# Performance work log

Measured on AMD Instinct MI355X. Metric: run time of the kernel, lower is better.

The kernel has to match this reference:

```python
import jax, jax.numpy as jnp
import numpy as np

N, E, D, R = 50000, 625000, 128, 200
BN_EPS = 1e-5


def setup_inputs() -> dict:
    key = jax.random.key(0)
    ks = jax.random.split(key, 16)
    x = jax.random.normal(ks[0], (N, D), dtype=jnp.float32)
    r_feats = jax.random.normal(ks[1], (R, D), dtype=jnp.float32)
    src = jax.random.randint(ks[2], (E,), 0, N, dtype=jnp.int32)
    dst = jax.random.randint(ks[3], (E,), 0, N, dtype=jnp.int32)
    etype = jax.random.randint(ks[4], (E,), 0, R, dtype=jnp.int32)
    norm = jax.random.uniform(ks[5], (E, 1), dtype=jnp.float32)
    out_edges_mask = jax.random.randint(ks[6], (E,), 0, 2) == 1
    in_edges_mask = jnp.logical_not(out_edges_mask)  # masks partition edges
    s = 1.0 / np.sqrt(D)
    def lin(k):
        kw, kb = jax.random.split(k)
        return (jax.random.uniform(kw, (D, D), jnp.float32, -s, s),
                jax.random.uniform(kb, (D,), jnp.float32, -s, s))
    W_O_w, W_O_b = lin(ks[7])
    W_I_w, W_I_b = lin(ks[8])
    W_S_w, W_S_b = lin(ks[9])
    W_R_w, W_R_b = lin(ks[10])
    loop_rel = jax.random.normal(ks[11], (1, D), dtype=jnp.float32) * s  # xavier-ish
    bn_gamma = jnp.ones((D,), jnp.float32)
    bn_beta = jnp.zeros((D,), jnp.float32)
    return {"x": x, "r_feats": r_feats, "src": src, "dst": dst, "etype": etype,
            "norm": norm, "in_edges_mask": in_edges_mask, "out_edges_mask": out_edges_mask,
            "W_O_w": W_O_w, "W_O_b": W_O_b, "W_I_w": W_I_w, "W_I_b": W_I_b,
            "W_S_w": W_S_w, "W_S_b": W_S_b, "W_R_w": W_R_w, "W_R_b": W_R_b,
            "loop_rel": loop_rel, "bn_gamma": bn_gamma, "bn_beta": bn_beta}


def reference(x, r_feats, src, dst, etype, norm, in_edges_mask, out_edges_mask,
              W_O_w, W_O_b, W_I_w, W_I_b, W_S_w, W_S_b, W_R_w, W_R_b,
              loop_rel, bn_gamma, bn_beta):
    # r_feats with self-loop relation appended: [R+1, D]
    r_ext = jnp.concatenate([r_feats, loop_rel], axis=0)
    # per-edge relation feature scaled by norm: [E, D]
    e_h = r_ext[etype] * norm
    # compose (sub): u_sub_e -> src feature minus edge feature
    comp_h = x[src] - e_h
    # per-direction linear projections, selected by the edge partition masks
    h_O = comp_h @ W_O_w.T + W_O_b
    h_I = comp_h @ W_I_w.T + W_I_b
    new_comp_h = jnp.where(out_edges_mask[:, None], h_O, h_I)
    # scatter-sum messages to destination nodes: [N, D]
    agg = jax.ops.segment_sum(new_comp_h, dst, num_segments=x.shape[0])
    # self-loop branch (sub with loop relation)
    comp_h_s = x - r_ext[-1]
    n_out = (comp_h_s @ W_S_w.T + W_S_b + agg) * (1.0 / 3.0)  # dropout in eval mode
    # BatchNorm1d (training-mode batch stats, biased variance)
    mean = jnp.mean(n_out, axis=0)
    var = jnp.mean((n_out - mean) ** 2, axis=0)
    n_out = (n_out - mean) * jax.lax.rsqrt(var + BN_EPS) * bn_gamma + bn_beta
    n_out = jnp.tanh(n_out)
    r_out = r_ext @ W_R_w.T + W_R_b
    return n_out, r_out[:-1]
```

## Files before the change

kernel.cpp:

```cpp
#include <hip/hip_runtime.h>
#include <cstddef>

#define N_NODES 50000
#define N_EDGES 625000
#define DIM     128
#define R_REL   200
#define BN_EPS  1e-5f
#define SLOTS   64
#define ND4     ((N_NODES * DIM) / 4)
#define R4      ((R_REL * DIM) / 4)

#define NB_FILL  2442
#define NB_CONV  3200
#define PREP_BASE (NB_FILL + NB_CONV)
#define NB_PREP  128
#define ROUT_BASE (PREP_BASE + NB_PREP)
#define NB_ROUT  100
#define NB_TOTAL (ROUT_BASE + NB_ROUT)

typedef __bf16 bf16x8 __attribute__((ext_vector_type(8)));
typedef float  f32x4  __attribute__((ext_vector_type(4)));

__device__ __forceinline__ float bfu2f(unsigned int hi16) {
    return __uint_as_float(hi16);
}
__device__ __forceinline__ unsigned int f2bfr(float f) {
    unsigned int u = __float_as_uint(f);
    return (u + 0x7fffu + ((u >> 16) & 1u)) >> 16;
}

__global__ __launch_bounds__(256) void init0_kernel(
    int* __restrict__ cnt,
    const unsigned char* __restrict__ in_m, const unsigned char* __restrict__ out_m,
    int* __restrict__ flag) {
    int gid = blockIdx.x * 256 + threadIdx.x;
    if (gid < N_NODES) cnt[gid] = 0;
    if (blockIdx.x == 0) {
        int ok = (((int)in_m[threadIdx.x] + (int)out_m[threadIdx.x]) == 1) ? 1 : 0;
        __shared__ int sred[4];
        unsigned long long b = __ballot(ok);
        if ((threadIdx.x & 63) == 0) sred[threadIdx.x >> 6] = (b == ~0ULL) ? 1 : 0;
        __syncthreads();
        if (threadIdx.x == 0) *flag = sred[0] & sred[1] & sred[2] & sred[3];
    }
}

__global__ __launch_bounds__(256) void fused_front_kernel(
    const int* __restrict__ dst, const int* __restrict__ src,
    const int* __restrict__ et, const float* __restrict__ norm,
    const void* __restrict__ omask, const int* __restrict__ flag,
    int* __restrict__ cnt, uint2* __restrict__ erec,
    const float* __restrict__ x, ushort* __restrict__ xb,
    const float* __restrict__ rf, ushort* __restrict__ rb,
    const float* __restrict__ WO, const float* __restrict__ WI,
    const float* __restrict__ WS, const float* __restrict__ loop,
    const float* __restrict__ bS, const float* __restrict__ bO,
    const float* __restrict__ bI, ushort* __restrict__ Wb,
    float* __restrict__ bias0, float* __restrict__ bO3, float* __restrict__ bI3,
    float* __restrict__ colsum, float* __restrict__ colsq,
    const float* __restrict__ WR, const float* __restrict__ bR,
    float* __restrict__ rout) {
    __shared__ float smem[256];
    int b = blockIdx.x, t = threadIdx.x;

    if (b < NB_FILL) {
        int e = b * 256 + t;
        if (e >= N_EDGES) return;
        int fl = *flag;
        bool m = fl ? (((const unsigned char*)omask)[e] != 0)
                    : (((const int*)omask)[e] != 0);
        int d = dst[e];
        int k = atomicAdd(&cnt[d], 1);
        if (k < SLOTS) {
            unsigned w0 = (unsigned)src[e] | ((unsigned)et[e] << 16) | (m ? 0x80000000u : 0u);
            erec[(size_t)d * SLOTS + k] = make_uint2(w0, (unsigned)__float_as_int(norm[e]));
        }
    } else if (b < PREP_BASE) {
        int cgid = (b - NB_FILL) * 256 + t;
        for (int i = cgid; i < ND4; i += NB_CONV * 256) {
            float4 v = ((const float4*)x)[i];
            ushort4 o;
            o.x = (ushort)f2bfr(v.x); o.y = (ushort)f2bfr(v.y);
            o.z = (ushort)f2bfr(v.z); o.w = (ushort)f2bfr(v.w);
            ((ushort4*)xb)[i] = o;
        }
        if (cgid < R4) {
            float4 v = ((const float4*)rf)[cgid];
            ushort4 o;
            o.x = (ushort)f2bfr(v.x); o.y = (ushort)f2bfr(v.y);
            o.z = (ushort)f2bfr(v.z); o.w = (ushort)f2bfr(v.w);
            ((ushort4*)rb)[cgid] = o;
        }
    } else if (b < ROUT_BASE) {
        int f = b - PREP_BASE;
        const float third = 1.0f / 3.0f;
        for (int k = t; k < 384; k += 256) {
            float w;
            if (k < 128)      w = WS[f * DIM + k];
            else if (k < 256) w = WO[f * DIM + (k - 128)];
            else              w = WI[f * DIM + (k - 256)];
            Wb[f * 384 + k] = (ushort)f2bfr(w * third);
        }
        if (t < 128) smem[t] = loop[t] * WS[f * DIM + t];
        __syncthreads();
        for (int off = 64; off; off >>= 1) {
            if (t < off) smem[t] += smem[t + off];
            __syncthreads();
        }
        if (t == 0) bias0[f] = (bS[f] - smem[0]) * third;
        if (t == 1) bO3[f] = bO[f] * third;
        if (t == 2) bI3[f] = bI[f] * third;
        if (f == 0 && t >= 128) { colsum[t - 128] = 0.f; colsq[t - 128] = 0.f; }
    } else {
        float* row2 = smem;
        int rloc = t >> 7, f = t & 127;
        int r = (b - ROUT_BASE) * 2 + rloc;
        row2[rloc * 128 + f] = rf[r * DIM + f];
        __syncthreads();
        float acc = bR[f];
        for (int k = 0; k < DIM; ++k) acc += row2[rloc * 128 + k] * WR[f * DIM + k];
        rout[r * DIM + f] = acc;
    }
}

#define AGG_CALC(EX, EY, XW, RW)                                   \
    {                                                              \
        float nm = __uint_as_float(EY);                            \
        float fm = (float)((EX) >> 31);                            \
        float x0 = bfu2f((XW) << 16), x1 = bfu2f((XW) & 0xffff0000u); \
        float r0 = bfu2f((RW) << 16), r1 = bfu2f((RW) & 0xffff0000u); \
        float v0 = __builtin_fmaf(-nm, r0, x0);                    \
        float v1 = __builtin_fmaf(-nm, r1, x1);                    \
        aT0 += v0; aT1 += v1;                                      \
        aO0 = __builtin_fmaf(fm, v0, aO0);                         \
        aO1 = __builtin_fmaf(fm, v1, aO1);                         \
        cOf += fm;                                                 \
    }

__global__ __launch_bounds__(256, 8) void aggregate_kernel(
    const unsigned int* __restrict__ xb,
    const unsigned int* __restrict__ rb,
    const uint2* __restrict__ erec,
    const int* __restrict__ cnt,
    unsigned int* __restrict__ S_Ob, unsigned int* __restrict__ S_Ib,
    float* __restrict__ cntO, float* __restrict__ cntI) {
    int wv = threadIdx.x >> 6;
    unsigned lane = threadIdx.x & 63;
    int n = blockIdx.x * 4 + wv;
    if (n >= N_NODES) return;
    int deg = cnt[n];
    deg = deg < SLOTS ? deg : SLOTS;
    int beg = n * SLOTS, end = beg + deg;

    float aT0 = 0.f, aT1 = 0.f, aO0 = 0.f, aO1 = 0.f, cOf = 0.f;

    int j = beg;
    for (; j + 7 < end; j += 8) {
        uint4 q01 = *(const uint4*)(erec + j);
        uint4 q23 = *(const uint4*)(erec + j + 2);
        uint4 q45 = *(const uint4*)(erec + j + 4);
        uint4 q67 = *(const uint4*)(erec + j + 6);
        unsigned xw0 = xb[((q01.x & 0xffffu) << 6) + lane];
        unsigned rw0 = rb[(((q01.x >> 16) & 0x7fffu) << 6) + lane];
        unsigned xw1 = xb[((q01.z & 0xffffu) << 6) + lane];
        unsigned rw1 = rb[(((q01.z >> 16) & 0x7fffu) << 6) + lane];
        unsigned xw2 = xb[((q23.x & 0xffffu) << 6) + lane];
        unsigned rw2 = rb[(((q23.x >> 16) & 0x7fffu) << 6) + lane];
        unsigned xw3 = xb[((q23.z & 0xffffu) << 6) + lane];
        unsigned rw3 = rb[(((q23.z >> 16) & 0x7fffu) << 6) + lane];
        unsigned xw4 = xb[((q45.x & 0xffffu) << 6) + lane];
        unsigned rw4 = rb[(((q45.x >> 16) & 0x7fffu) << 6) + lane];
        unsigned xw5 = xb[((q45.z & 0xffffu) << 6) + lane];
        unsigned rw5 = rb[(((q45.z >> 16) & 0x7fffu) << 6) + lane];
        unsigned xw6 = xb[((q67.x & 0xffffu) << 6) + lane];
        unsigned rw6 = rb[(((q67.x >> 16) & 0x7fffu) << 6) + lane];
        unsigned xw7 = xb[((q67.z & 0xffffu) << 6) + lane];
        unsigned rw7 = rb[(((q67.z >> 16) & 0x7fffu) << 6) + lane];
        AGG_CALC(q01.x, q01.y, xw0, rw0)
        AGG_CALC(q01.z, q01.w, xw1, rw1)
        AGG_CALC(q23.x, q23.y, xw2, rw2)
        AGG_CALC(q23.z, q23.w, xw3, rw3)
        AGG_CALC(q45.x, q45.y, xw4, rw4)
        AGG_CALC(q45.z, q45.w, xw5, rw5)
        AGG_CALC(q67.x, q67.y, xw6, rw6)
        AGG_CALC(q67.z, q67.w, xw7, rw7)
    }
    if (j + 3 < end) {
        uint4 q01 = *(const uint4*)(erec + j);
        uint4 q23 = *(const uint4*)(erec + j + 2);
        unsigned xw0 = xb[((q01.x & 0xffffu) << 6) + lane];
        unsigned rw0 = rb[(((q01.x >> 16) & 0x7fffu) << 6) + lane];
        unsigned xw1 = xb[((q01.z & 0xffffu) << 6) + lane];
        unsigned rw1 = rb[(((q01.z >> 16) & 0x7fffu) << 6) + lane];
        unsigned xw2 = xb[((q23.x & 0xffffu) << 6) + lane];
        unsigned rw2 = rb[(((q23.x >> 16) & 0x7fffu) << 6) + lane];
        unsigned xw3 = xb[((q23.z & 0xffffu) << 6) + lane];
        unsigned rw3 = rb[(((q23.z >> 16) & 0x7fffu) << 6) + lane];
        AGG_CALC(q01.x, q01.y, xw0, rw0)
        AGG_CALC(q01.z, q01.w, xw1, rw1)
        AGG_CALC(q23.x, q23.y, xw2, rw2)
        AGG_CALC(q23.z, q23.w, xw3, rw3)
        j += 4;
    }
    if (j + 1 < end) {
        uint4 q01 = *(const uint4*)(erec + j);
        unsigned xw0 = xb[((q01.x & 0xffffu) << 6) + lane];
        unsigned rw0 = rb[(((q01.x >> 16) & 0x7fffu) << 6) + lane];
        unsigned xw1 = xb[((q01.z & 0xffffu) << 6) + lane];
        unsigned rw1 = rb[(((q01.z >> 16) & 0x7fffu) << 6) + lane];
        AGG_CALC(q01.x, q01.y, xw0, rw0)
        AGG_CALC(q01.z, q01.w, xw1, rw1)
        j += 2;
    }
    if (j < end) {
        uint2 e0 = erec[j];
        unsigned xw0 = xb[((e0.x & 0xffffu) << 6) + lane];
        unsigned rw0 = rb[(((e0.x >> 16) & 0x7fffu) << 6) + lane];
        AGG_CALC(e0.x, e0.y, xw0, rw0)
    }

    float aI0 = aT0 - aO0, aI1 = aT1 - aO1;
    S_Ob[((unsigned)n << 6) + lane] = f2bfr(aO0) | (f2bfr(aO1) << 16);
    S_Ib[((unsigned)n << 6) + lane] = f2bfr(aI0) | (f2bfr(aI1) << 16);
    if (lane == 0) { cntO[n] = cOf; cntI[n] = (float)deg - cOf; }
}

__global__ __launch_bounds__(256, 4) void gemm_kernel(
    const ushort* __restrict__ xb, const ushort* __restrict__ S_Ob,
    const ushort* __restrict__ S_Ib, const ushort* __restrict__ Wb,
    const float* __restrict__ bias0, const float* __restrict__ bO3,
    const float* __restrict__ bI3, const float* __restrict__ cntO,
    const float* __restrict__ cntI, float* __restrict__ y,
    float* __restrict__ colsum, float* __restrict__ colsq) {
    __shared__ ushort Bs[128][136];
    __shared__ float redS[4][128];
    __shared__ float redQ[4][128];

    int tid = threadIdx.x;
    int wv = tid >> 6, lane = tid & 63;
    int cl = lane & 15, kg = lane >> 4;
    int wrow0 = blockIdx.x * 64 + wv * 16;

    f32x4 acc[8];
#pragma unroll
    for (int cf = 0; cf < 8; ++cf) acc[cf] = (f32x4){0.f, 0.f, 0.f, 0.f};

    int rowA = wrow0 + cl;
    int rowc = rowA < N_NODES ? rowA : N_NODES - 1;
    const ushort* Abase[3] = {xb, S_Ob, S_Ib};

    for (int kq = 0; kq < 3; ++kq) {
        __syncthreads();
#pragma unroll
        for (int j = 0; j < 8; ++j) {
            int i = tid + j * 256;
            int col = i >> 4, k8 = (i & 15) << 3;
            uint4 w = *(const uint4*)(Wb + (size_t)col * 384 + kq * 128 + k8);
            *(uint4*)&Bs[col][k8] = w;
        }
        const ushort* Ap0 = Abase[kq] + (size_t)rowc * 128 + kg * 8;
        uint4 a4[4];
#pragma unroll
        for (int ks = 0; ks < 4; ++ks) a4[ks] = *(const uint4*)(Ap0 + ks * 32);
        __syncthreads();
#pragma unroll
        for (int ks = 0; ks < 4; ++ks) {
            bf16x8 af = __builtin_bit_cast(bf16x8, a4[ks]);
#pragma unroll
            for (int cf = 0; cf < 8; ++cf) {
                bf16x8 bv = __builtin_bit_cast(bf16x8,
                    *(const uint4*)&Bs[cf * 16 + cl][ks * 32 + kg * 8]);
                acc[cf] = __builtin_amdgcn_mfma_f32_16x16x32_bf16(af, bv, acc[cf], 0, 0, 0);
            }
        }
    }

    float b0a[8], boa[8], bia[8];
#pragma unroll
    for (int cf = 0; cf < 8; ++cf) {
        int col = cf * 16 + cl;
        b0a[cf] = bias0[col]; boa[cf] = bO3[col]; bia[cf] = bI3[col];
    }
    float cOv[4], cIv[4]; int rows[4]; bool rv[4];
#pragma unroll
    for (int r = 0; r < 4; ++r) {
        int row = wrow0 + kg * 4 + r;
        rows[r] = row; rv[r] = row < N_NODES;
        cOv[r] = rv[r] ? cntO[row] : 0.f;
        cIv[r] = rv[r] ? cntI[row] : 0.f;
    }
    float ps[8], pq[8];
#pragma unroll
    for (int cf = 0; cf < 8; ++cf) {
        float s = 0.f, q = 0.f;
        int col = cf * 16 + cl;
#pragma unroll
        for (int r = 0; r < 4; ++r) {
            if (rv[r]) {
                float v = acc[cf][r] + b0a[cf] + cOv[r] * boa[cf] + cIv[r] * bia[cf];
                y[(size_t)rows[r] * DIM + col] = v;
                s += v; q += v * v;
            }
        }
        s += __shfl_xor(s, 16);
        s += __shfl_xor(s, 32);
        q += __shfl_xor(q, 16);
        q += __shfl_xor(q, 32);
        ps[cf] = s; pq[cf] = q;
    }
    if (kg == 0) {
#pragma unroll
        for (int cf = 0; cf < 8; ++cf) {
            redS[wv][cf * 16 + cl] = ps[cf];
            redQ[wv][cf * 16 + cl] = pq[cf];
        }
    }
    __syncthreads();
    if (tid < 128) {
        float s = redS[0][tid] + redS[1][tid] + redS[2][tid] + redS[3][tid];
        float q = redQ[0][tid] + redQ[1][tid] + redQ[2][tid] + redQ[3][tid];
        atomicAdd(colsum + tid, s);
        atomicAdd(colsq + tid, q);
    }
}

__global__ __launch_bounds__(256) void bn_apply_kernel(
    float* __restrict__ y, const float* __restrict__ colsum, const float* __restrict__ colsq,
    const float* __restrict__ gamma, const float* __restrict__ beta) {
    __shared__ __align__(16) float sc[DIM];
    __shared__ __align__(16) float sh[DIM];
    int tid = threadIdx.x;
    if (tid < DIM) {
        float mean = colsum[tid] * (1.0f / N_NODES);
        float var  = colsq[tid] * (1.0f / N_NODES) - mean * mean;
        float s = rsqrtf(var + BN_EPS) * gamma[tid];
        sc[tid] = s;
        sh[tid] = beta[tid] - mean * s;
    }
    __syncthreads();
    const int total4 = N_NODES * 32;
    for (int i = blockIdx.x * 256 + tid; i < total4; i += gridDim.x * 256) {
        float4 s4 = ((const float4*)sc)[i & 31];
        float4 h4 = ((const float4*)sh)[i & 31];
        float4 v = ((float4*)y)[i];
        v.x = tanhf(v.x * s4.x + h4.x);
        v.y = tanhf(v.y * s4.y + h4.y);
        v.z = tanhf(v.z * s4.z + h4.z);
        v.w = tanhf(v.w * s4.w + h4.w);
        ((float4*)y)[i] = v;
    }
}

extern "C" void kernel_launch(void* const* d_in, const int* in_sizes, int n_in,
                              void* d_out, int out_size, void* d_ws, size_t ws_size,
                              hipStream_t stream) {
    const float* x        = (const float*)d_in[0];
    const float* r_feats  = (const float*)d_in[1];
    const int*   src      = (const int*)d_in[2];
    const int*   dst      = (const int*)d_in[3];
    const int*   etype    = (const int*)d_in[4];
    const float* norm     = (const float*)d_in[5];
    const void*  in_mask  = d_in[6];
    const void*  out_mask = d_in[7];
    const float* W_O_w    = (const float*)d_in[8];
    const float* W_O_b    = (const float*)d_in[9];
    const float* W_I_w    = (const float*)d_in[10];
    const float* W_I_b    = (const float*)d_in[11];
    const float* W_S_w    = (const float*)d_in[12];
    const float* W_S_b    = (const float*)d_in[13];
    const float* W_R_w    = (const float*)d_in[14];
    const float* W_R_b    = (const float*)d_in[15];
    const float* loop_rel = (const float*)d_in[16];
    const float* bn_gamma = (const float*)d_in[17];
    const float* bn_beta  = (const float*)d_in[18];

    const size_t ND = (size_t)N_NODES * DIM;
    char* p = (char*)d_ws;
    auto alloc = [&](size_t bytes) { void* r = (void*)p; p += (bytes + 255) & ~(size_t)255; return r; };

    ushort* S_Ob = (ushort*)alloc(ND * 2);
    ushort* S_Ib = (ushort*)alloc(ND * 2);
    ushort* xb   = (ushort*)alloc(ND * 2);
    ushort* rb   = (ushort*)alloc((size_t)R_REL * DIM * 2);
    uint2* erec  = (uint2*)alloc((size_t)N_NODES * SLOTS * 8);
    ushort* Wb   = (ushort*)alloc((size_t)DIM * 384 * 2);
    float* bias0 = (float*)alloc(DIM * 4);
    float* bO3   = (float*)alloc(DIM * 4);
    float* bI3   = (float*)alloc(DIM * 4);
    float* colsum= (float*)alloc(DIM * 4);
    float* colsq = (float*)alloc(DIM * 4);
    float* cntO  = (float*)alloc(N_NODES * 4);
    float* cntI  = (float*)alloc(N_NODES * 4);
    int*   cnt   = (int*)alloc(N_NODES * 4);
    int*   flag  = (int*)alloc(4);

    float* y    = (float*)d_out;
    float* rout = (float*)d_out + ND;

    init0_kernel<<<(N_NODES + 255) / 256, 256, 0, stream>>>(
        cnt, (const unsigned char*)in_mask, (const unsigned char*)out_mask, flag);

    fused_front_kernel<<<NB_TOTAL, 256, 0, stream>>>(
        dst, src, etype, norm, out_mask, flag, cnt, erec,
        x, xb, r_feats, rb,
        W_O_w, W_I_w, W_S_w, loop_rel, W_S_b, W_O_b, W_I_b,
        Wb, bias0, bO3, bI3, colsum, colsq,
        W_R_w, W_R_b, rout);

    aggregate_kernel<<<(N_NODES + 3) / 4, 256, 0, stream>>>(
        (const unsigned int*)xb, (const unsigned int*)rb, erec, cnt,
        (unsigned int*)S_Ob, (unsigned int*)S_Ib, cntO, cntI);

    gemm_kernel<<<(N_NODES + 63) / 64, 256, 0, stream>>>(
        xb, S_Ob, S_Ib, Wb, bias0, bO3, bI3, cntO, cntI, y, colsum, colsq);

    bn_apply_kernel<<<2048, 256, 0, stream>>>(y, colsum, colsq, bn_gamma, bn_beta);
}
```

Before: 129.5 us.

## Fuse BatchNorm apply into GEMM via grid-wide barrier, keeping outputs in registers

Merges the BN-apply kernel into the GEMM kernel. Each block keeps its pre-norm outputs in accumulator registers, adds its column sums atomically, then spins on a global completion counter until all 782 blocks finish, computes scale and shift, and writes tanh outputs once. This removes the 25.6 MB write and re-read of y and one kernel launch. The cost is a software grid barrier, which relies on all 782 blocks being co-resident (4 blocks per CU at 256 threads) and would deadlock otherwise. Blocks also idle while waiting for the slowest one.

```diff
diff --git a/kernel.cpp b/kernel.cpp
--- a/kernel.cpp
+++ b/kernel.cpp
@@ -9,6 +9,7 @@
 #define SLOTS   64
 #define ND4     ((N_NODES * DIM) / 4)
 #define R4      ((R_REL * DIM) / 4)
+#define NBLK_GEMM 782
 
 #define NB_FILL  2442
 #define NB_CONV  3200
@@ -30,11 +31,12 @@
 }
 
 __global__ __launch_bounds__(256) void init0_kernel(
-    int* __restrict__ cnt,
+    int* __restrict__ cnt, int* __restrict__ done,
     const unsigned char* __restrict__ in_m, const unsigned char* __restrict__ out_m,
     int* __restrict__ flag) {
     int gid = blockIdx.x * 256 + threadIdx.x;
     if (gid < N_NODES) cnt[gid] = 0;
+    if (gid == 0) *done = 0;
     if (blockIdx.x == 0) {
         int ok = (((int)in_m[threadIdx.x] + (int)out_m[threadIdx.x]) == 1) ? 1 : 0;
         __shared__ int sred[4];
@@ -225,16 +227,20 @@
     if (lane == 0) { cntO[n] = cOf; cntI[n] = (float)deg - cOf; }
 }
 
-__global__ __launch_bounds__(256, 4) void gemm_kernel(
+__global__ __launch_bounds__(256, 4) void gemm_bn_kernel(
     const ushort* __restrict__ xb, const ushort* __restrict__ S_Ob,
     const ushort* __restrict__ S_Ib, const ushort* __restrict__ Wb,
     const float* __restrict__ bias0, const float* __restrict__ bO3,
     const float* __restrict__ bI3, const float* __restrict__ cntO,
     const float* __restrict__ cntI, float* __restrict__ y,
-    float* __restrict__ colsum, float* __restrict__ colsq) {
+    float* __restrict__ colsum, float* __restrict__ colsq,
+    int* __restrict__ done,
+    const float* __restrict__ gamma, const float* __restrict__ beta) {
     __shared__ ushort Bs[128][136];
-    __shared__ float redS[4][128];
-    __shared__ float redQ[4][128];
+    float* redS = (float*)&Bs[0][0];
+    float* redQ = redS + 512;
+    float* scs  = redQ + 512;
+    float* shs  = scs + 128;
 
     int tid = threadIdx.x;
     int wv = tid >> 6, lane = tid & 63;
@@ -275,12 +281,6 @@
         }
     }
 
-    float b0a[8], boa[8], bia[8];
-#pragma unroll
-    for (int cf = 0; cf < 8; ++cf) {
-        int col = cf * 16 + cl;
-        b0a[cf] = bias0[col]; boa[cf] = bO3[col]; bia[cf] = bI3[col];
-    }
     float cOv[4], cIv[4]; int rows[4]; bool rv[4];
 #pragma unroll
     for (int r = 0; r < 4; ++r) {
@@ -294,11 +294,12 @@
     for (int cf = 0; cf < 8; ++cf) {
         float s = 0.f, q = 0.f;
         int col = cf * 16 + cl;
+        float b0v = bias0[col], bov = bO3[col], biv = bI3[col];
 #pragma unroll
         for (int r = 0; r < 4; ++r) {
             if (rv[r]) {
-                float v = acc[cf][r] + b0a[cf] + cOv[r] * boa[cf] + cIv[r] * bia[cf];
-                y[(size_t)rows[r] * DIM + col] = v;
+                float v = acc[cf][r] + b0v + cOv[r] * bov + cIv[r] * biv;
+                acc[cf][r] = v;
                 s += v; q += v * v;
             }
         }
@@ -308,46 +309,52 @@
         q += __shfl_xor(q, 32);
         ps[cf] = s; pq[cf] = q;
     }
+    __syncthreads();
     if (kg == 0) {
 #pragma unroll
         for (int cf = 0; cf < 8; ++cf) {
-            redS[wv][cf * 16 + cl] = ps[cf];
-            redQ[wv][cf * 16 + cl] = pq[cf];
+            redS[wv * 128 + cf * 16 + cl] = ps[cf];
+            redQ[wv * 128 + cf * 16 + cl] = pq[cf];
         }
     }
     __syncthreads();
     if (tid < 128) {
-        float s = redS[0][tid] + redS[1][tid] + redS[2][tid] + redS[3][tid];
-        float q = redQ[0][tid] + redQ[1][tid] + redQ[2][tid] + redQ[3][tid];
+        float s = redS[tid] + redS[128 + tid] + redS[256 + tid] + redS[384 + tid];
+        float q = redQ[tid] + redQ[128 + tid] + redQ[256 + tid] + redQ[384 + tid];
         atomicAdd(colsum + tid, s);
         atomicAdd(colsq + tid, q);
     }
-}
-
-__global__ __launch_bounds__(256) void bn_apply_kernel(
-    float* __restrict__ y, const float* __restrict__ colsum, const float* __restrict__ colsq,
-    const float* __restrict__ gamma, const float* __restrict__ beta) {
-    __shared__ __align__(16) float sc[DIM];
-    __shared__ __align__(16) float sh[DIM];
-    int tid = threadIdx.x;
-    if (tid < DIM) {
-        float mean = colsum[tid] * (1.0f / N_NODES);
-        float var  = colsq[tid] * (1.0f / N_NODES) - mean * mean;
-        float s = rsqrtf(var + BN_EPS) * gamma[tid];
-        sc[tid] = s;
-        sh[tid] = beta[tid] - mean * s;
-    }
     __syncthreads();
-    const int total4 = N_NODES * 32;
-    for (int i = blockIdx.x * 256 + tid; i < total4; i += gridDim.x * 256) {
-        float4 s4 = ((const float4*)sc)[i & 31];
-        float4 h4 = ((const float4*)sh)[i & 31];
-        float4 v = ((float4*)y)[i];
-        v.x = tanhf(v.x * s4.x + h4.x);
-        v.y = tanhf(v.y * s4.y + h4.y);
-        v.z = tanhf(v.z * s4.z + h4.z);
-        v.w = tanhf(v.w * s4.w + h4.w);
-        ((float4*)y)[i] = v;
+
+    if (tid == 0) {
+        __hip_atomic_fetch_add(done, 1, __ATOMIC_RELEASE, __HIP_MEMORY_SCOPE_AGENT);
+        while (__hip_atomic_load(done, __ATOMIC_ACQUIRE, __HIP_MEMORY_SCOPE_AGENT)
+               < NBLK_GEMM) { __builtin_amdgcn_s_sleep(8); }
+    }
+    __syncthreads();
+
+    if (tid < 128) {
+        float cs = __hip_atomic_load(&colsum[tid], __ATOMIC_RELAXED,
+                                     __HIP_MEMORY_SCOPE_AGENT);
+        float cq = __hip_atomic_load(&colsq[tid], __ATOMIC_RELAXED,
+                                     __HIP_MEMORY_SCOPE_AGENT);
+        float mean = cs * (1.0f / N_NODES);
+        float var  = cq * (1.0f / N_NODES) - mean * mean;
+        float sc = rsqrtf(var + BN_EPS) * gamma[tid];
+        scs[tid] = sc;
+        shs[tid] = beta[tid] - mean * sc;
+    }
+    __syncthreads();
+#pragma unroll
+    for (int cf = 0; cf < 8; ++cf) {
+        int col = cf * 16 + cl;
+        float sc = scs[col], sh = shs[col];
+#pragma unroll
+        for (int r = 0; r < 4; ++r) {
+            if (rv[r]) {
+                y[(size_t)rows[r] * DIM + col] = tanhf(acc[cf][r] * sc + sh);
+            }
+        }
     }
 }
 
@@ -393,12 +400,13 @@
     float* cntI  = (float*)alloc(N_NODES * 4);
     int*   cnt   = (int*)alloc(N_NODES * 4);
     int*   flag  = (int*)alloc(4);
+    int*   done  = (int*)alloc(4);
 
     float* y    = (float*)d_out;
     float* rout = (float*)d_out + ND;
 
     init0_kernel<<<(N_NODES + 255) / 256, 256, 0, stream>>>(
-        cnt, (const unsigned char*)in_mask, (const unsigned char*)out_mask, flag);
+        cnt, done, (const unsigned char*)in_mask, (const unsigned char*)out_mask, flag);
 
     fused_front_kernel<<<NB_TOTAL, 256, 0, stream>>>(
         dst, src, etype, norm, out_mask, flag, cnt, erec,
@@ -411,8 +419,7 @@
         (const unsigned int*)xb, (const unsigned int*)rb, erec, cnt,
         (unsigned int*)S_Ob, (unsigned int*)S_Ib, cntO, cntI);
 
-    gemm_kernel<<<(N_NODES + 63) / 64, 256, 0, stream>>>(
-        xb, S_Ob, S_Ib, Wb, bias0, bO3, bI3, cntO, cntI, y, colsum, colsq);
-
-    bn_apply_kernel<<<2048, 256, 0, stream>>>(y, colsum, colsq, bn_gamma, bn_beta);
-}
+    gemm_bn_kernel<<<NBLK_GEMM, 256, 0, stream>>>(
+        xb, S_Ob, S_Ib, Wb, bias0, bO3, bI3, cntO, cntI, y, colsum, colsq,
+        done, bn_gamma, bn_beta);
+}
```

Measured after the change: 200.1 us. +54.5%, slower.
